# Performance work log

Measured on AMD Instinct MI355X. Metric: run time of the kernel, lower is better.

## Reference

```python
import jax, jax.numpy as jnp
import numpy as np

K = 16      # knn neighbors (init kwarg k)
EPS = 1e-5  # batch-norm eps


def setup_inputs() -> dict:
    key = jax.random.key(0)
    ks = jax.random.split(key, 4)
    B, N, C, O = 16, 2048, 16, 64
    x = jax.random.normal(ks[0], (B * N, C), dtype=jnp.float32)
    batch = jnp.repeat(jnp.arange(B, dtype=jnp.int32), N)  # sorted equal-size graphs
    W1 = jax.random.normal(ks[1], (2 * C, O), dtype=jnp.float32) * (1.0 / np.sqrt(2 * C))
    b1 = jnp.zeros((O,), jnp.float32)
    g1 = jnp.ones((O,), jnp.float32)
    be1 = jnp.zeros((O,), jnp.float32)
    Wg = jax.random.normal(ks[2], (O, 1), dtype=jnp.float32) * (1.0 / np.sqrt(O))
    bg = jnp.zeros((1,), jnp.float32)
    gg = jnp.ones((1,), jnp.float32)
    beg = jnp.zeros((1,), jnp.float32)
    return {"x": x, "batch": batch, "W1": W1, "b1": b1, "g1": g1, "be1": be1,
            "Wg": Wg, "bg": bg, "gg": gg, "beg": beg, "num_graphs": B}


def reference(x, batch, W1, b1, g1, be1, Wg, bg, gg, beg, num_graphs):
    B = int(num_graphs)
    total, C = x.shape
    N = total // B
    xb = x.reshape(B, N, C)

    # --- dynamic kNN graph in feature space (per graph in the batch) ---
    sq = jnp.sum(xb * xb, axis=-1)                                   # [B,N]
    d = sq[:, :, None] + sq[:, None, :] - 2.0 * jnp.einsum('bnc,bmc->bnm', xb, xb)
    _, idx = jax.lax.top_k(-d, K)                                    # [B,N,K], includes self (d=0)

    # --- edge features: cat([x_i, x_j - x_i]) ---
    xj = jax.vmap(lambda pts, ids: pts[ids])(xb, idx)                # [B,N,K,C]
    xi = jnp.broadcast_to(xb[:, :, None, :], xj.shape)               # [B,N,K,C]
    e = jnp.concatenate([xi, xj - xi], axis=-1)                      # [B,N,K,2C]

    # --- edge MLP: Linear -> BatchNorm(train stats) -> SiLU ---
    h = e @ W1 + b1                                                  # [B,N,K,O]
    mu = h.mean(axis=(0, 1, 2))
    var = h.var(axis=(0, 1, 2))
    h = jax.nn.silu((h - mu) / jnp.sqrt(var + EPS) * g1 + be1)

    # --- attentional aggregation: gate MLP -> softmax over k edges -> weighted sum ---
    gt = h @ Wg + bg                                                 # [B,N,K,1]
    gmu = gt.mean()
    gvar = gt.var()
    gt = jax.nn.silu((gt - gmu) / jnp.sqrt(gvar + EPS) * gg + beg)
    a = jax.nn.softmax(gt, axis=2)                                   # softmax over K per target node
    out = jnp.sum(a * h, axis=2)                                     # [B,N,O]
    return out.reshape(total, -1)
```

## Files before the change

### kernel.cpp

```cpp
#include <hip/hip_runtime.h>
#include <math.h>
#include <float.h>

#define BGRAPH 16
#define NPTS   2048
#define CDIM   16
#define ODIM   64
#define KNN    16
#define NTOT   (BGRAPH*NPTS)
#define NEDGE  (NTOT*KNN)
#define EPSBN  1e-5f
#define NBLK_E 2048
#define NPW    4
#define NSETS  16


__global__ __launch_bounds__(256) void pq_kernel(
    const float* __restrict__ x, const float* __restrict__ W1,
    const float* __restrict__ b1,
    float* __restrict__ P, float* __restrict__ Q, float* __restrict__ sq,
    float* __restrict__ abuf) {
  if (blockIdx.x == 0) {
    for (int t = threadIdx.x; t < NSETS*128 + 2*NSETS; t += 256) abuf[t] = 0.f;
  }
  int lane = threadIdx.x & 63;
  int nin  = threadIdx.x >> 6;
  int node = blockIdx.x * 4 + nin;
  __shared__ float xs[4][CDIM];
  if (threadIdx.x < 4*CDIM) {
    int n = threadIdx.x / CDIM, c = threadIdx.x % CDIM;
    xs[n][c] = x[(blockIdx.x*4 + n)*CDIM + c];
  }
  __syncthreads();
  float p = 0.f, q = b1[lane];
  #pragma unroll
  for (int c = 0; c < CDIM; ++c) {
    float xv = xs[nin][c];
    float wb = W1[(c+CDIM)*ODIM + lane];
    float wa = W1[c*ODIM + lane];
    p += xv * wb;
    q += xv * (wa - wb);
  }
  P[node*ODIM + lane] = p;
  Q[node*ODIM + lane] = q;
  if (lane == 0) {
    float s = 0.f;
    #pragma unroll
    for (int c = 0; c < CDIM; ++c) { float xv = xs[nin][c]; s += xv*xv; }
    sq[node] = s;
  }
}

#define KROWS 8
__device__ __forceinline__ unsigned long long packkey(float dv, int j) {
  unsigned ub = __float_as_uint(dv);
  ub ^= ((unsigned)((int)ub >> 31)) | 0x80000000u;
  return (((unsigned long long)ub) << 32) | (unsigned)j;
}
__device__ __forceinline__ float rfl(float v) {
  return __uint_as_float(__builtin_amdgcn_readfirstlane(__float_as_uint(v)));
}

__global__ __launch_bounds__(256, 3) void knn_kernel(
    const float* __restrict__ x, const float* __restrict__ sq,
    int* __restrict__ idxOut) {
  __shared__ float sT16[CDIM][256];
  __shared__ float dB[32][256];
  __shared__ unsigned long long skey[4][64];
  __shared__ int scnt[4];
  const int tid  = threadIdx.x;
  const int lane = tid & 63;
  const int w    = tid >> 6;
  const int blocksPerGraph = NPTS / KROWS;
  const int g     = blockIdx.x / blocksPerGraph;
  const int rb    = (blockIdx.x % blocksPerGraph) * KROWS;
  const int gbase = g * NPTS;
  const int r0    = rb + w*2;

  float ta[CDIM], tb[CDIM]; float tsqA, tsqB;
  {
    const float4* tp = (const float4*)(x + (size_t)(gbase + r0)*CDIM);
    float4 t0 = tp[0], t1 = tp[1], t2 = tp[2], t3 = tp[3];
    ta[0]=rfl(t0.x);  ta[1]=rfl(t0.y);  ta[2]=rfl(t0.z);  ta[3]=rfl(t0.w);
    ta[4]=rfl(t1.x);  ta[5]=rfl(t1.y);  ta[6]=rfl(t1.z);  ta[7]=rfl(t1.w);
    ta[8]=rfl(t2.x);  ta[9]=rfl(t2.y);  ta[10]=rfl(t2.z); ta[11]=rfl(t2.w);
    ta[12]=rfl(t3.x); ta[13]=rfl(t3.y); ta[14]=rfl(t3.z); ta[15]=rfl(t3.w);
    tsqA = rfl(sq[gbase + r0]);
    const float4* up = (const float4*)(x + (size_t)(gbase + r0 + 1)*CDIM);
    float4 u0 = up[0], u1 = up[1], u2 = up[2], u3 = up[3];
    tb[0]=rfl(u0.x);  tb[1]=rfl(u0.y);  tb[2]=rfl(u0.z);  tb[3]=rfl(u0.w);
    tb[4]=rfl(u1.x);  tb[5]=rfl(u1.y);  tb[6]=rfl(u1.z);  tb[7]=rfl(u1.w);
    tb[8]=rfl(u2.x);  tb[9]=rfl(u2.y);  tb[10]=rfl(u2.z); tb[11]=rfl(u2.w);
    tb[12]=rfl(u3.x); tb[13]=rfl(u3.y); tb[14]=rfl(u3.z); tb[15]=rfl(u3.w);
    tsqB = rfl(sq[gbase + r0 + 1]);
  }

  float d[32];

  float4 a0, a1, a2, a3;
  {
    const float4* xp = (const float4*)(x + (size_t)(gbase + tid)*CDIM);
    a0 = xp[0]; a1 = xp[1]; a2 = xp[2]; a3 = xp[3];
  }

  #pragma unroll
  for (int t = 0; t < NPTS/256; ++t) {
    __syncthreads();
    sT16[0][tid]=a0.x;  sT16[1][tid]=a0.y;  sT16[2][tid]=a0.z;  sT16[3][tid]=a0.w;
    sT16[4][tid]=a1.x;  sT16[5][tid]=a1.y;  sT16[6][tid]=a1.z;  sT16[7][tid]=a1.w;
    sT16[8][tid]=a2.x;  sT16[9][tid]=a2.y;  sT16[10][tid]=a2.z; sT16[11][tid]=a2.w;
    sT16[12][tid]=a3.x; sT16[13][tid]=a3.y; sT16[14][tid]=a3.z; sT16[15][tid]=a3.w;
    __syncthreads();
    if (t < NPTS/256 - 1) {
      const float4* xp = (const float4*)(x + (size_t)(gbase + (t+1)*256 + tid)*CDIM);
      a0 = xp[0]; a1 = xp[1]; a2 = xp[2]; a3 = xp[3];
    }

    float4 sq4 = *(const float4*)(sq + gbase + t*256 + 4*lane);
    float sqv[4] = {sq4.x, sq4.y, sq4.z, sq4.w};

    float dotA[4] = {0.f,0.f,0.f,0.f};
    float dotB[4] = {0.f,0.f,0.f,0.f};
    #pragma unroll
    for (int c = 0; c < CDIM; ++c) {
      float4 cv = *(const float4*)(&sT16[c][4*lane]);
      float xa = ta[c], xb = tb[c];
      dotA[0] += xa*cv.x; dotA[1] += xa*cv.y; dotA[2] += xa*cv.z; dotA[3] += xa*cv.w;
      dotB[0] += xb*cv.x; dotB[1] += xb*cv.y; dotB[2] += xb*cv.z; dotB[3] += xb*cv.w;
    }
    #pragma unroll
    for (int rr = 0; rr < 4; ++rr) {
      d[t*4 + rr] = tsqA + sqv[rr] - 2.f*dotA[rr];
      dB[t*4 + rr][tid] = tsqB + sqv[rr] - 2.f*dotB[rr];
    }
  }

  {
    float lmin = d[0];
    #pragma unroll
    for (int s = 1; s < 32; ++s) lmin = fminf(lmin, d[s]);

    float v = lmin;
    #pragma unroll
    for (int k = 2; k <= 64; k <<= 1) {
      #pragma unroll
      for (int j = k >> 1; j > 0; j >>= 1) {
        float o = __shfl_xor(v, j);
        bool asc   = ((lane & k) == 0);
        bool lower = ((lane & j) == 0);
        float mn = fminf(v, o), mx = fmaxf(v, o);
        v = (asc == lower) ? mn : mx;
      }
    }
    float T = __shfl(v, 15);

    if (lane == 0) scnt[w] = 0;
    #pragma unroll
    for (int s = 0; s < 32; ++s) {
      if (d[s] <= T) {
        int p = atomicAdd(&scnt[w], 1);
        if (p < 64) {
          int j = (s >> 2)*256 + 4*lane + (s & 3);
          skey[w][p] = packkey(d[s], j);
        }
      }
    }
    int M = scnt[w];
    int row = gbase + r0;

    if (M <= 64) {
      unsigned long long key = (lane < M) ? skey[w][lane] : ~0ull;
      #pragma unroll
      for (int k = 2; k <= 64; k <<= 1) {
        #pragma unroll
        for (int j = k >> 1; j > 0; j >>= 1) {
          unsigned long long o = __shfl_xor(key, j);
          bool asc   = ((lane & k) == 0);
          bool lower = ((lane & j) == 0);
          unsigned long long mn = (key < o) ? key : o;
          unsigned long long mx = (key < o) ? o : key;
          key = (asc == lower) ? mn : mx;
        }
      }
      if (lane < KNN)
        idxOut[(size_t)row*KNN + lane] = gbase + (int)(key & 0xffffffffu);
    } else {
      for (int sel = 0; sel < KNN; ++sel) {
        unsigned long long lb = ~0ull;
        #pragma unroll
        for (int s = 0; s < 32; ++s) {
          int j = (s >> 2)*256 + 4*lane + (s & 3);
          unsigned long long ks = packkey(d[s], j);
          if (ks < lb) lb = ks;
        }
        #pragma unroll
        for (int off = 32; off > 0; off >>= 1) {
          unsigned long long o = __shfl_xor(lb, off);
          if (o < lb) lb = o;
        }
        if (lane == 0)
          idxOut[(size_t)row*KNN + sel] = gbase + (int)(lb & 0xffffffffu);
        #pragma unroll
        for (int s = 0; s < 32; ++s) {
          int j = (s >> 2)*256 + 4*lane + (s & 3);
          if (packkey(d[s], j) == lb) d[s] = FLT_MAX;
        }
      }
    }
  }

  {
    float lmin = dB[0][tid];
    #pragma unroll
    for (int s = 1; s < 32; ++s) lmin = fminf(lmin, dB[s][tid]);

    float v = lmin;
    #pragma unroll
    for (int k = 2; k <= 64; k <<= 1) {
      #pragma unroll
      for (int j = k >> 1; j > 0; j >>= 1) {
        float o = __shfl_xor(v, j);
        bool asc   = ((lane & k) == 0);
        bool lower = ((lane & j) == 0);
        float mn = fminf(v, o), mx = fmaxf(v, o);
        v = (asc == lower) ? mn : mx;
      }
    }
    float T = __shfl(v, 15);

    if (lane == 0) scnt[w] = 0;
    #pragma unroll
    for (int s = 0; s < 32; ++s) {
      float dv = dB[s][tid];
      if (dv <= T) {
        int p = atomicAdd(&scnt[w], 1);
        if (p < 64) {
          int j = (s >> 2)*256 + 4*lane + (s & 3);
          skey[w][p] = packkey(dv, j);
        }
      }
    }
    int M = scnt[w];
    int row = gbase + r0 + 1;

    if (M <= 64) {
      unsigned long long key = (lane < M) ? skey[w][lane] : ~0ull;
      #pragma unroll
      for (int k = 2; k <= 64; k <<= 1) {
        #pragma unroll
        for (int j = k >> 1; j > 0; j >>= 1) {
          unsigned long long o = __shfl_xor(key, j);
          bool asc   = ((lane & k) == 0);
          bool lower = ((lane & j) == 0);
          unsigned long long mn = (key < o) ? key : o;
          unsigned long long mx = (key < o) ? o : key;
          key = (asc == lower) ? mn : mx;
        }
      }
      if (lane < KNN)
        idxOut[(size_t)row*KNN + lane] = gbase + (int)(key & 0xffffffffu);
    } else {
      for (int sel = 0; sel < KNN; ++sel) {
        unsigned long long lb = ~0ull;
        #pragma unroll
        for (int s = 0; s < 32; ++s) {
          int j = (s >> 2)*256 + 4*lane + (s & 3);
          unsigned long long ks = packkey(dB[s][tid], j);
          if (ks < lb) lb = ks;
        }
        #pragma unroll
        for (int off = 32; off > 0; off >>= 1) {
          unsigned long long o = __shfl_xor(lb, off);
          if (o < lb) lb = o;
        }
        if (lane == 0)
          idxOut[(size_t)row*KNN + sel] = gbase + (int)(lb & 0xffffffffu);
        #pragma unroll
        for (int s = 0; s < 32; ++s) {
          int j = (s >> 2)*256 + 4*lane + (s & 3);
          if (packkey(dB[s][tid], j) == lb) dB[s][tid] = FLT_MAX;
        }
      }
    }
  }
}

__global__ __launch_bounds__(256, 4) void stats1a_kernel(
    const float* __restrict__ P, const float* __restrict__ Q,
    const int* __restrict__ idx, float* __restrict__ abuf) {
  int tid  = threadIdx.x;
  int lane = tid & 63;
  int wid  = tid >> 6;
  int grp  = lane >> 4;
  int p    = lane & 15;
  int gw   = blockIdx.x * 4 + wid;
  int n0 = gw * NPW;
  float4 q4v[NPW]; int4 j4v[NPW];
  #pragma unroll
  for (int ii = 0; ii < NPW; ++ii) {
    int i = n0 + ii;
    q4v[ii] = *(const float4*)(Q + (size_t)i*ODIM + 4*p);
    j4v[ii] = *(const int4*)(idx + (size_t)i*KNN + 4*grp);
  }
  float4 s4  = {0.f,0.f,0.f,0.f};
  float4 ss4 = {0.f,0.f,0.f,0.f};
  #pragma unroll
  for (int ii = 0; ii < NPW; ++ii) {
    float4 q4 = q4v[ii];
    float4 v0 = *(const float4*)(P + (size_t)j4v[ii].x*ODIM + 4*p);
    float4 v1 = *(const float4*)(P + (size_t)j4v[ii].y*ODIM + 4*p);
    float4 v2 = *(const float4*)(P + (size_t)j4v[ii].z*ODIM + 4*p);
    float4 v3 = *(const float4*)(P + (size_t)j4v[ii].w*ODIM + 4*p);
    {
      float hx=q4.x+v0.x, hy=q4.y+v0.y, hz=q4.z+v0.z, hw=q4.w+v0.w;
      s4.x+=hx; s4.y+=hy; s4.z+=hz; s4.w+=hw;
      ss4.x+=hx*hx; ss4.y+=hy*hy; ss4.z+=hz*hz; ss4.w+=hw*hw;
    }
    {
      float hx=q4.x+v1.x, hy=q4.y+v1.y, hz=q4.z+v1.z, hw=q4.w+v1.w;
      s4.x+=hx; s4.y+=hy; s4.z+=hz; s4.w+=hw;
      ss4.x+=hx*hx; ss4.y+=hy*hy; ss4.z+=hz*hz; ss4.w+=hw*hw;
    }
    {
      float hx=q4.x+v2.x, hy=q4.y+v2.y, hz=q4.z+v2.z, hw=q4.w+v2.w;
      s4.x+=hx; s4.y+=hy; s4.z+=hz; s4.w+=hw;
      ss4.x+=hx*hx; ss4.y+=hy*hy; ss4.z+=hz*hz; ss4.w+=hw*hw;
    }
    {
      float hx=q4.x+v3.x, hy=q4.y+v3.y, hz=q4.z+v3.z, hw=q4.w+v3.w;
      s4.x+=hx; s4.y+=hy; s4.z+=hz; s4.w+=hw;
      ss4.x+=hx*hx; ss4.y+=hy*hy; ss4.z+=hz*hz; ss4.w+=hw*hw;
    }
  }
  s4.x  += __shfl_xor(s4.x,16);  s4.x  += __shfl_xor(s4.x,32);
  s4.y  += __shfl_xor(s4.y,16);  s4.y  += __shfl_xor(s4.y,32);
  s4.z  += __shfl_xor(s4.z,16);  s4.z  += __shfl_xor(s4.z,32);
  s4.w  += __shfl_xor(s4.w,16);  s4.w  += __shfl_xor(s4.w,32);
  ss4.x += __shfl_xor(ss4.x,16); ss4.x += __shfl_xor(ss4.x,32);
  ss4.y += __shfl_xor(ss4.y,16); ss4.y += __shfl_xor(ss4.y,32);
  ss4.z += __shfl_xor(ss4.z,16); ss4.z += __shfl_xor(ss4.z,32);
  ss4.w += __shfl_xor(ss4.w,16); ss4.w += __shfl_xor(ss4.w,32);
  __shared__ float ls[4][ODIM], lss[4][ODIM];
  if (grp == 0) {
    *(float4*)&ls[wid][4*p]  = s4;
    *(float4*)&lss[wid][4*p] = ss4;
  }
  __syncthreads();
  if (tid < 2*ODIM) {
    float a;
    if (tid < ODIM) a = ls[0][tid] + ls[1][tid] + ls[2][tid] + ls[3][tid];
    else { int o = tid - ODIM; a = lss[0][o] + lss[1][o] + lss[2][o] + lss[3][o]; }
    atomicAdd(&abuf[(blockIdx.x & (NSETS-1))*128 + tid], a);
  }
}

__global__ __launch_bounds__(256, 4) void stats2a_kernel(
    const float* __restrict__ P, const float* __restrict__ Q,
    const int* __restrict__ idx,
    const float* __restrict__ g1, const float* __restrict__ be1,
    const float* __restrict__ Wg, const float* __restrict__ bg,
    const float* __restrict__ abuf, float* __restrict__ scale,
    float* __restrict__ shift, float* __restrict__ gtbuf,
    float* __restrict__ gacc) {
  int tid  = threadIdx.x;
  int lane = tid & 63;
  int wid  = tid >> 6;
  int grp  = lane >> 4;
  int p    = lane & 15;
  int gw   = blockIdx.x * 4 + wid;
  int n0 = gw * NPW;
  float4 q4v[NPW]; int4 j4v[NPW];
  #pragma unroll
  for (int ii = 0; ii < NPW; ++ii) {
    int i = n0 + ii;
    q4v[ii] = *(const float4*)(Q + (size_t)i*ODIM + 4*p);
    j4v[ii] = *(const int4*)(idx + (size_t)i*KNN + 4*grp);
  }
  __shared__ __align__(16) float s_sc[ODIM], s_sh[ODIM];
  __shared__ float red[2*ODIM];
  if (tid < 2*ODIM) {
    float a = 0.f;
    #pragma unroll
    for (int t = 0; t < NSETS; ++t) a += abuf[t*128 + tid];
    red[tid] = a;
  }
  __syncthreads();
  if (tid < ODIM) {
    float mu  = red[tid] / (float)NEDGE;
    float var = red[ODIM+tid] / (float)NEDGE - mu*mu;
    float inv = 1.0f / sqrtf(var + EPSBN);
    float sc = g1[tid] * inv;
    float sh = be1[tid] - mu * sc;
    s_sc[tid] = sc; s_sh[tid] = sh;
    if (blockIdx.x == 0) { scale[tid] = sc; shift[tid] = sh; }
  }
  __syncthreads();

  float4 sc4 = *(const float4*)&s_sc[4*p];
  float4 sh4 = *(const float4*)&s_sh[4*p];
  float4 wg4 = *(const float4*)(Wg + 4*p);
  float bgv = bg[0];
  float s = 0.f, ss = 0.f;
  #pragma unroll
  for (int ii = 0; ii < NPW; ++ii) {
    int i = n0 + ii;
    float4 q4 = q4v[ii];
    float4 pv[4];
    pv[0] = *(const float4*)(P + (size_t)j4v[ii].x*ODIM + 4*p);
    pv[1] = *(const float4*)(P + (size_t)j4v[ii].y*ODIM + 4*p);
    pv[2] = *(const float4*)(P + (size_t)j4v[ii].z*ODIM + 4*p);
    pv[3] = *(const float4*)(P + (size_t)j4v[ii].w*ODIM + 4*p);
    #pragma unroll
    for (int e = 0; e < 4; ++e) {
      float4 p4 = pv[e];
      float zx = (q4.x + p4.x)*sc4.x + sh4.x;
      float zy = (q4.y + p4.y)*sc4.y + sh4.y;
      float zz = (q4.z + p4.z)*sc4.z + sh4.z;
      float zw = (q4.w + p4.w)*sc4.w + sh4.w;
      float v = (zx/(1.f+expf(-zx)))*wg4.x
              + (zy/(1.f+expf(-zy)))*wg4.y
              + (zz/(1.f+expf(-zz)))*wg4.z
              + (zw/(1.f+expf(-zw)))*wg4.w;
      v += __shfl_xor(v, 1);
      v += __shfl_xor(v, 2);
      v += __shfl_xor(v, 4);
      v += __shfl_xor(v, 8);
      float gt = v + bgv;
      if (p == 0) gtbuf[(size_t)i*KNN + 4*grp + e] = gt;
      s += gt; ss += gt*gt;
    }
  }
  s  += __shfl_xor(s, 16);  s  += __shfl_xor(s, 32);
  ss += __shfl_xor(ss, 16); ss += __shfl_xor(ss, 32);
  __shared__ float pw[4], pws[4];
  if (lane == 0) { pw[wid] = s; pws[wid] = ss; }
  __syncthreads();
  if (tid == 0) {
    int set = blockIdx.x & (NSETS-1);
    atomicAdd(&gacc[2*set],   pw[0]+pw[1]+pw[2]+pw[3]);
    atomicAdd(&gacc[2*set+1], pws[0]+pws[1]+pws[2]+pws[3]);
  }
}

__global__ __launch_bounds__(256, 4) void final_kernel(
    const float* __restrict__ P, const float* __restrict__ Q,
    const int* __restrict__ idx, const float* __restrict__ scale,
    const float* __restrict__ shift, const float* __restrict__ gtbuf,
    const float* __restrict__ gacc, const float* __restrict__ gg,
    const float* __restrict__ beg, float* __restrict__ out) {
  __shared__ float g2[2];
  if (threadIdx.x == 0) {
    float S = 0.f, SS = 0.f;
    #pragma unroll
    for (int t = 0; t < NSETS; ++t) { S += gacc[2*t]; SS += gacc[2*t+1]; }
    float mu  = S / (float)NEDGE;
    float var = SS / (float)NEDGE - mu*mu;
    float inv = 1.f / sqrtf(var + EPSBN);
    float sg = gg[0] * inv;
    g2[0] = sg; g2[1] = beg[0] - mu * sg;
  }
  __syncthreads();
  int lane = threadIdx.x & 63;
  int wid  = threadIdx.x >> 6;
  int grp  = lane >> 4;
  int p    = lane & 15;
  int iA = blockIdx.x * 8 + wid * 2;
  int iB = iA + 1;
  float4 sc4 = *(const float4*)(scale + 4*p);
  float4 sh4 = *(const float4*)(shift + 4*p);
  float gscale = g2[0], gshift = g2[1];
  float4 qA = *(const float4*)(Q + (size_t)iA*ODIM + 4*p);
  float4 qB = *(const float4*)(Q + (size_t)iB*ODIM + 4*p);
  int4   jA = *(const int4*)(idx + (size_t)iA*KNN + 4*grp);
  int4   jB = *(const int4*)(idx + (size_t)iB*KNN + 4*grp);
  float4 gA = *(const float4*)(gtbuf + (size_t)iA*KNN + 4*grp);
  float4 gB = *(const float4*)(gtbuf + (size_t)iB*KNN + 4*grp);
  float4 pA0 = *(const float4*)(P + (size_t)jA.x*ODIM + 4*p);
  float4 pA1 = *(const float4*)(P + (size_t)jA.y*ODIM + 4*p);
  float4 pA2 = *(const float4*)(P + (size_t)jA.z*ODIM + 4*p);
  float4 pA3 = *(const float4*)(P + (size_t)jA.w*ODIM + 4*p);
  float4 pB0 = *(const float4*)(P + (size_t)jB.x*ODIM + 4*p);
  float4 pB1 = *(const float4*)(P + (size_t)jB.y*ODIM + 4*p);
  float4 pB2 = *(const float4*)(P + (size_t)jB.z*ODIM + 4*p);
  float4 pB3 = *(const float4*)(P + (size_t)jB.w*ODIM + 4*p);

  {
    float z0 = gA.x*gscale + gshift, z1 = gA.y*gscale + gshift;
    float z2 = gA.z*gscale + gshift, z3 = gA.w*gscale + gshift;
    float gt0 = z0/(1.f+expf(-z0)), gt1 = z1/(1.f+expf(-z1));
    float gt2 = z2/(1.f+expf(-z2)), gt3 = z3/(1.f+expf(-z3));
    float m = fmaxf(fmaxf(gt0, gt1), fmaxf(gt2, gt3));
    m = fmaxf(m, __shfl_xor(m, 16));
    m = fmaxf(m, __shfl_xor(m, 32));
    float e0 = expf(gt0-m), e1 = expf(gt1-m), e2 = expf(gt2-m), e3 = expf(gt3-m);
    float se = e0+e1+e2+e3;
    se += __shfl_xor(se, 16);
    se += __shfl_xor(se, 32);
    float invs = 1.f / se;
    float a0 = e0*invs, a1 = e1*invs, a2 = e2*invs, a3 = e3*invs;
    float4 acc = {0.f,0.f,0.f,0.f};
    {
      float zx=(qA.x+pA0.x)*sc4.x+sh4.x, zy=(qA.y+pA0.y)*sc4.y+sh4.y;
      float zz=(qA.z+pA0.z)*sc4.z+sh4.z, zw=(qA.w+pA0.w)*sc4.w+sh4.w;
      acc.x += a0*(zx/(1.f+expf(-zx))); acc.y += a0*(zy/(1.f+expf(-zy)));
      acc.z += a0*(zz/(1.f+expf(-zz))); acc.w += a0*(zw/(1.f+expf(-zw)));
    }
    {
      float zx=(qA.x+pA1.x)*sc4.x+sh4.x, zy=(qA.y+pA1.y)*sc4.y+sh4.y;
      float zz=(qA.z+pA1.z)*sc4.z+sh4.z, zw=(qA.w+pA1.w)*sc4.w+sh4.w;
      acc.x += a1*(zx/(1.f+expf(-zx))); acc.y += a1*(zy/(1.f+expf(-zy)));
      acc.z += a1*(zz/(1.f+expf(-zz))); acc.w += a1*(zw/(1.f+expf(-zw)));
    }
    {
      float zx=(qA.x+pA2.x)*sc4.x+sh4.x, zy=(qA.y+pA2.y)*sc4.y+sh4.y;
      float zz=(qA.z+pA2.z)*sc4.z+sh4.z, zw=(qA.w+pA2.w)*sc4.w+sh4.w;
      acc.x += a2*(zx/(1.f+expf(-zx))); acc.y += a2*(zy/(1.f+expf(-zy)));
      acc.z += a2*(zz/(1.f+expf(-zz))); acc.w += a2*(zw/(1.f+expf(-zw)));
    }
    {
      float zx=(qA.x+pA3.x)*sc4.x+sh4.x, zy=(qA.y+pA3.y)*sc4.y+sh4.y;
      float zz=(qA.z+pA3.z)*sc4.z+sh4.z, zw=(qA.w+pA3.w)*sc4.w+sh4.w;
      acc.x += a3*(zx/(1.f+expf(-zx))); acc.y += a3*(zy/(1.f+expf(-zy)));
      acc.z += a3*(zz/(1.f+expf(-zz))); acc.w += a3*(zw/(1.f+expf(-zw)));
    }
    acc.x += __shfl_xor(acc.x,16); acc.x += __shfl_xor(acc.x,32);
    acc.y += __shfl_xor(acc.y,16); acc.y += __shfl_xor(acc.y,32);
    acc.z += __shfl_xor(acc.z,16); acc.z += __shfl_xor(acc.z,32);
    acc.w += __shfl_xor(acc.w,16); acc.w += __shfl_xor(acc.w,32);
    if (grp == 0)
      *(float4*)(out + (size_t)iA*ODIM + 4*p) = acc;
  }

  {
    float z0 = gB.x*gscale + gshift, z1 = gB.y*gscale + gshift;
    float z2 = gB.z*gscale + gshift, z3 = gB.w*gscale + gshift;
    float gt0 = z0/(1.f+expf(-z0)), gt1 = z1/(1.f+expf(-z1));
    float gt2 = z2/(1.f+expf(-z2)), gt3 = z3/(1.f+expf(-z3));
    float m = fmaxf(fmaxf(gt0, gt1), fmaxf(gt2, gt3));
    m = fmaxf(m, __shfl_xor(m, 16));
    m = fmaxf(m, __shfl_xor(m, 32));
    float e0 = expf(gt0-m), e1 = expf(gt1-m), e2 = expf(gt2-m), e3 = expf(gt3-m);
    float se = e0+e1+e2+e3;
    se += __shfl_xor(se, 16);
    se += __shfl_xor(se, 32);
    float invs = 1.f / se;
    float a0 = e0*invs, a1 = e1*invs, a2 = e2*invs, a3 = e3*invs;
    float4 acc = {0.f,0.f,0.f,0.f};
    {
      float zx=(qB.x+pB0.x)*sc4.x+sh4.x, zy=(qB.y+pB0.y)*sc4.y+sh4.y;
      float zz=(qB.z+pB0.z)*sc4.z+sh4.z, zw=(qB.w+pB0.w)*sc4.w+sh4.w;
      acc.x += a0*(zx/(1.f+expf(-zx))); acc.y += a0*(zy/(1.f+expf(-zy)));
      acc.z += a0*(zz/(1.f+expf(-zz))); acc.w += a0*(zw/(1.f+expf(-zw)));
    }
    {
      float zx=(qB.x+pB1.x)*sc4.x+sh4.x, zy=(qB.y+pB1.y)*sc4.y+sh4.y;
      float zz=(qB.z+pB1.z)*sc4.z+sh4.z, zw=(qB.w+pB1.w)*sc4.w+sh4.w;
      acc.x += a1*(zx/(1.f+expf(-zx))); acc.y += a1*(zy/(1.f+expf(-zy)));
      acc.z += a1*(zz/(1.f+expf(-zz))); acc.w += a1*(zw/(1.f+expf(-zw)));
    }
    {
      float zx=(qB.x+pB2.x)*sc4.x+sh4.x, zy=(qB.y+pB2.y)*sc4.y+sh4.y;
      float zz=(qB.z+pB2.z)*sc4.z+sh4.z, zw=(qB.w+pB2.w)*sc4.w+sh4.w;
      acc.x += a2*(zx/(1.f+expf(-zx))); acc.y += a2*(zy/(1.f+expf(-zy)));
      acc.z += a2*(zz/(1.f+expf(-zz))); acc.w += a2*(zw/(1.f+expf(-zw)));
    }
    {
      float zx=(qB.x+pB3.x)*sc4.x+sh4.x, zy=(qB.y+pB3.y)*sc4.y+sh4.y;
      float zz=(qB.z+pB3.z)*sc4.z+sh4.z, zw=(qB.w+pB3.w)*sc4.w+sh4.w;
      acc.x += a3*(zx/(1.f+expf(-zx))); acc.y += a3*(zy/(1.f+expf(-zy)));
      acc.z += a3*(zz/(1.f+expf(-zz))); acc.w += a3*(zw/(1.f+expf(-zw)));
    }
    acc.x += __shfl_xor(acc.x,16); acc.x += __shfl_xor(acc.x,32);
    acc.y += __shfl_xor(acc.y,16); acc.y += __shfl_xor(acc.y,32);
    acc.z += __shfl_xor(acc.z,16); acc.z += __shfl_xor(acc.z,32);
    acc.w += __shfl_xor(acc.w,16); acc.w += __shfl_xor(acc.w,32);
    if (grp == 0)
      *(float4*)(out + (size_t)iB*ODIM + 4*p) = acc;
  }
}

extern "C" void kernel_launch(void* const* d_in, const int* in_sizes, int n_in,
                              void* d_out, int out_size, void* d_ws, size_t ws_size,
                              hipStream_t stream) {
  const float* x   = (const float*)d_in[0];
  const float* W1  = (const float*)d_in[2];
  const float* b1  = (const float*)d_in[3];
  const float* g1  = (const float*)d_in[4];
  const float* be1 = (const float*)d_in[5];
  const float* Wg  = (const float*)d_in[6];
  const float* bg  = (const float*)d_in[7];
  const float* gg  = (const float*)d_in[8];
  const float* beg = (const float*)d_in[9];
  float* out = (float*)d_out;

  char* ws = (char*)d_ws;
  int*   idx   = (int*)  (ws);
  float* P     = (float*)(ws + 2097152);
  float* Q     = (float*)(ws + 10485760);
  float* sq    = (float*)(ws + 18874368);
  float* abuf  = (float*)(ws + 19005440);
  float* gacc  = abuf + NSETS*128;
  float* gtbuf = (float*)(ws + 20070400);
  float* scale = (float*)(ws + 22167552);
  float* shift = (float*)(ws + 22167808);

  pq_kernel<<<NTOT/4, 256, 0, stream>>>(x, W1, b1, P, Q, sq, abuf);
  knn_kernel<<<NTOT/KROWS, 256, 0, stream>>>(x, sq, idx);
  stats1a_kernel<<<NBLK_E, 256, 0, stream>>>(P, Q, idx, abuf);
  stats2a_kernel<<<NBLK_E, 256, 0, stream>>>(P, Q, idx, g1, be1, Wg, bg, abuf, scale, shift, gtbuf, gacc);
  final_kernel<<<NTOT/8, 256, 0, stream>>>(P, Q, idx, scale, shift, gtbuf, gacc, gg, beg, out);
}
```

Measured before the change: 270.1 us.

## Fuse first-pass edge BatchNorm statistics into the kNN kernel epilogue

The separate stats1a kernel is removed. Its per-feature sum and sum-of-squares accumulation now runs at the end of knn_kernel, on the same rows each wave just selected neighbours for. The neighbour indices are read back right after they are written, which saves one kernel launch and a separate pass over idx, and the cross-wave combine reuses the dB shared buffer. In exchange, knn blocks do extra gather work, which adds latency and register pressure to an already heavy kernel.

```diff
diff --git a/kernel.cpp b/kernel.cpp
--- a/kernel.cpp
+++ b/kernel.cpp
@@ -63,7 +63,8 @@
 
 __global__ __launch_bounds__(256, 3) void knn_kernel(
     const float* __restrict__ x, const float* __restrict__ sq,
-    int* __restrict__ idxOut) {
+    const float* __restrict__ P, const float* __restrict__ Q,
+    int* __restrict__ idxOut, float* __restrict__ abuf) {
   __shared__ float sT16[CDIM][256];
   __shared__ float dB[32][256];
   __shared__ unsigned long long skey[4][64];
@@ -283,74 +284,65 @@
       }
     }
   }
-}
-
-__global__ __launch_bounds__(256, 4) void stats1a_kernel(
-    const float* __restrict__ P, const float* __restrict__ Q,
-    const int* __restrict__ idx, float* __restrict__ abuf) {
-  int tid  = threadIdx.x;
-  int lane = tid & 63;
-  int wid  = tid >> 6;
-  int grp  = lane >> 4;
-  int p    = lane & 15;
-  int gw   = blockIdx.x * 4 + wid;
-  int n0 = gw * NPW;
-  float4 q4v[NPW]; int4 j4v[NPW];
-  #pragma unroll
-  for (int ii = 0; ii < NPW; ++ii) {
-    int i = n0 + ii;
-    q4v[ii] = *(const float4*)(Q + (size_t)i*ODIM + 4*p);
-    j4v[ii] = *(const int4*)(idx + (size_t)i*KNN + 4*grp);
-  }
-  float4 s4  = {0.f,0.f,0.f,0.f};
-  float4 ss4 = {0.f,0.f,0.f,0.f};
-  #pragma unroll
-  for (int ii = 0; ii < NPW; ++ii) {
-    float4 q4 = q4v[ii];
-    float4 v0 = *(const float4*)(P + (size_t)j4v[ii].x*ODIM + 4*p);
-    float4 v1 = *(const float4*)(P + (size_t)j4v[ii].y*ODIM + 4*p);
-    float4 v2 = *(const float4*)(P + (size_t)j4v[ii].z*ODIM + 4*p);
-    float4 v3 = *(const float4*)(P + (size_t)j4v[ii].w*ODIM + 4*p);
-    {
-      float hx=q4.x+v0.x, hy=q4.y+v0.y, hz=q4.z+v0.z, hw=q4.w+v0.w;
-      s4.x+=hx; s4.y+=hy; s4.z+=hz; s4.w+=hw;
-      ss4.x+=hx*hx; ss4.y+=hy*hy; ss4.z+=hz*hz; ss4.w+=hw*hw;
-    }
-    {
-      float hx=q4.x+v1.x, hy=q4.y+v1.y, hz=q4.z+v1.z, hw=q4.w+v1.w;
-      s4.x+=hx; s4.y+=hy; s4.z+=hz; s4.w+=hw;
-      ss4.x+=hx*hx; ss4.y+=hy*hy; ss4.z+=hz*hz; ss4.w+=hw*hw;
-    }
-    {
-      float hx=q4.x+v2.x, hy=q4.y+v2.y, hz=q4.z+v2.z, hw=q4.w+v2.w;
-      s4.x+=hx; s4.y+=hy; s4.z+=hz; s4.w+=hw;
-      ss4.x+=hx*hx; ss4.y+=hy*hy; ss4.z+=hz*hz; ss4.w+=hw*hw;
-    }
-    {
-      float hx=q4.x+v3.x, hy=q4.y+v3.y, hz=q4.z+v3.z, hw=q4.w+v3.w;
-      s4.x+=hx; s4.y+=hy; s4.z+=hz; s4.w+=hw;
-      ss4.x+=hx*hx; ss4.y+=hy*hy; ss4.z+=hz*hz; ss4.w+=hw*hw;
-    }
-  }
-  s4.x  += __shfl_xor(s4.x,16);  s4.x  += __shfl_xor(s4.x,32);
-  s4.y  += __shfl_xor(s4.y,16);  s4.y  += __shfl_xor(s4.y,32);
-  s4.z  += __shfl_xor(s4.z,16);  s4.z  += __shfl_xor(s4.z,32);
-  s4.w  += __shfl_xor(s4.w,16);  s4.w  += __shfl_xor(s4.w,32);
-  ss4.x += __shfl_xor(ss4.x,16); ss4.x += __shfl_xor(ss4.x,32);
-  ss4.y += __shfl_xor(ss4.y,16); ss4.y += __shfl_xor(ss4.y,32);
-  ss4.z += __shfl_xor(ss4.z,16); ss4.z += __shfl_xor(ss4.z,32);
-  ss4.w += __shfl_xor(ss4.w,16); ss4.w += __shfl_xor(ss4.w,32);
-  __shared__ float ls[4][ODIM], lss[4][ODIM];
-  if (grp == 0) {
-    *(float4*)&ls[wid][4*p]  = s4;
-    *(float4*)&lss[wid][4*p] = ss4;
-  }
+
   __syncthreads();
-  if (tid < 2*ODIM) {
-    float a;
-    if (tid < ODIM) a = ls[0][tid] + ls[1][tid] + ls[2][tid] + ls[3][tid];
-    else { int o = tid - ODIM; a = lss[0][o] + lss[1][o] + lss[2][o] + lss[3][o]; }
-    atomicAdd(&abuf[(blockIdx.x & (NSETS-1))*128 + tid], a);
+  {
+    const int grp = lane >> 4;
+    const int p   = lane & 15;
+    float4 s4  = {0.f,0.f,0.f,0.f};
+    float4 ss4 = {0.f,0.f,0.f,0.f};
+    #pragma unroll
+    for (int rp = 0; rp < 2; ++rp) {
+      int row = gbase + r0 + rp;
+      float4 q4 = *(const float4*)(Q + (size_t)row*ODIM + 4*p);
+      int4 j4 = *(const int4*)(idxOut + (size_t)row*KNN + 4*grp);
+      float4 v0 = *(const float4*)(P + (size_t)j4.x*ODIM + 4*p);
+      float4 v1 = *(const float4*)(P + (size_t)j4.y*ODIM + 4*p);
+      float4 v2 = *(const float4*)(P + (size_t)j4.z*ODIM + 4*p);
+      float4 v3 = *(const float4*)(P + (size_t)j4.w*ODIM + 4*p);
+      {
+        float hx=q4.x+v0.x, hy=q4.y+v0.y, hz=q4.z+v0.z, hw=q4.w+v0.w;
+        s4.x+=hx; s4.y+=hy; s4.z+=hz; s4.w+=hw;
+        ss4.x+=hx*hx; ss4.y+=hy*hy; ss4.z+=hz*hz; ss4.w+=hw*hw;
+      }
+      {
+        float hx=q4.x+v1.x, hy=q4.y+v1.y, hz=q4.z+v1.z, hw=q4.w+v1.w;
+        s4.x+=hx; s4.y+=hy; s4.z+=hz; s4.w+=hw;
+        ss4.x+=hx*hx; ss4.y+=hy*hy; ss4.z+=hz*hz; ss4.w+=hw*hw;
+      }
+      {
+        float hx=q4.x+v2.x, hy=q4.y+v2.y, hz=q4.z+v2.z, hw=q4.w+v2.w;
+        s4.x+=hx; s4.y+=hy; s4.z+=hz; s4.w+=hw;
+        ss4.x+=hx*hx; ss4.y+=hy*hy; ss4.z+=hz*hz; ss4.w+=hw*hw;
+      }
+      {
+        float hx=q4.x+v3.x, hy=q4.y+v3.y, hz=q4.z+v3.z, hw=q4.w+v3.w;
+        s4.x+=hx; s4.y+=hy; s4.z+=hz; s4.w+=hw;
+        ss4.x+=hx*hx; ss4.y+=hy*hy; ss4.z+=hz*hz; ss4.w+=hw*hw;
+      }
+    }
+    s4.x  += __shfl_xor(s4.x,16);  s4.x  += __shfl_xor(s4.x,32);
+    s4.y  += __shfl_xor(s4.y,16);  s4.y  += __shfl_xor(s4.y,32);
+    s4.z  += __shfl_xor(s4.z,16);  s4.z  += __shfl_xor(s4.z,32);
+    s4.w  += __shfl_xor(s4.w,16);  s4.w  += __shfl_xor(s4.w,32);
+    ss4.x += __shfl_xor(ss4.x,16); ss4.x += __shfl_xor(ss4.x,32);
+    ss4.y += __shfl_xor(ss4.y,16); ss4.y += __shfl_xor(ss4.y,32);
+    ss4.z += __shfl_xor(ss4.z,16); ss4.z += __shfl_xor(ss4.z,32);
+    ss4.w += __shfl_xor(ss4.w,16); ss4.w += __shfl_xor(ss4.w,32);
+    float* comb = &dB[0][0];
+    if (grp == 0) {
+      *(float4*)&comb[w*ODIM + 4*p]       = s4;
+      *(float4*)&comb[256 + w*ODIM + 4*p] = ss4;
+    }
+    __syncthreads();
+    if (tid < ODIM) {
+      float a = comb[tid] + comb[64+tid] + comb[128+tid] + comb[192+tid];
+      atomicAdd(&abuf[(blockIdx.x & (NSETS-1))*128 + tid], a);
+    } else if (tid < 2*ODIM) {
+      int o = tid - ODIM;
+      float a = comb[256+o] + comb[256+64+o] + comb[256+128+o] + comb[256+192+o];
+      atomicAdd(&abuf[(blockIdx.x & (NSETS-1))*128 + tid], a);
+    }
   }
 }
 
@@ -605,8 +597,7 @@
   float* shift = (float*)(ws + 22167808);
 
   pq_kernel<<<NTOT/4, 256, 0, stream>>>(x, W1, b1, P, Q, sq, abuf);
-  knn_kernel<<<NTOT/KROWS, 256, 0, stream>>>(x, sq, idx);
-  stats1a_kernel<<<NBLK_E, 256, 0, stream>>>(P, Q, idx, abuf);
+  knn_kernel<<<NTOT/KROWS, 256, 0, stream>>>(x, sq, P, Q, idx, abuf);
   stats2a_kernel<<<NBLK_E, 256, 0, stream>>>(P, Q, idx, g1, be1, Wg, bg, abuf, scale, shift, gtbuf, gacc);
   final_kernel<<<NTOT/8, 256, 0, stream>>>(P, Q, idx, scale, shift, gtbuf, gacc, gg, beg, out);
 }
```

Result: no change. 268.8 us (-0.5%).
